# Kernel optimization log

Measured on AMD Instinct MI355X. Metric: run time of the kernel, lower is better.

The kernel has to match this reference:

```python
import jax, jax.numpy as jnp
import numpy as np

QLEN, MLEN, BSZ = 1024, 1024, 4
D_MODEL, N_HEAD, D_HEAD, D_INNER = 1024, 16, 64, 4096
KLEN = QLEN + MLEN  # = rlen
LN_EPS = 1e-5


def setup_inputs() -> dict:
    key = jax.random.key(0)
    ks = jax.random.split(key, 16)
    s = 0.02
    nhd = N_HEAD * D_HEAD
    inp = {
        "dec_inp": jax.random.normal(ks[0], (QLEN, BSZ, D_MODEL), jnp.float32),
        "r": jax.random.normal(ks[1], (KLEN, D_MODEL), jnp.float32),
        "r_w_bias": jax.random.normal(ks[2], (N_HEAD, D_HEAD), jnp.float32) * s,
        "r_r_bias": jax.random.normal(ks[3], (N_HEAD, D_HEAD), jnp.float32) * s,
        "mems": jax.random.normal(ks[4], (MLEN, BSZ, D_MODEL), jnp.float32),
        # causal mask with memory: position j visible to query i iff j <= i + MLEN
        "dec_attn_mask": (jnp.arange(KLEN)[None, :] > (jnp.arange(QLEN)[:, None] + MLEN))[:, :, None],
        # parameters
        "qkv_w": jax.random.normal(ks[5], (D_MODEL, 3 * nhd), jnp.float32) * s,
        "r_w": jax.random.normal(ks[6], (D_MODEL, nhd), jnp.float32) * s,
        "o_w": jax.random.normal(ks[7], (nhd, D_MODEL), jnp.float32) * s,
        "ln1_w": jnp.ones((D_MODEL,), jnp.float32),
        "ln1_b": jnp.zeros((D_MODEL,), jnp.float32),
        "ln2_w": jnp.ones((D_MODEL,), jnp.float32),
        "ln2_b": jnp.zeros((D_MODEL,), jnp.float32),
        "ff_w1": jax.random.normal(ks[8], (D_MODEL, D_INNER), jnp.float32) * s,
        "ff_b1": jnp.zeros((D_INNER,), jnp.float32),
        "ff_w2": jax.random.normal(ks[9], (D_INNER, D_MODEL), jnp.float32) * s,
        "ff_b2": jnp.zeros((D_MODEL,), jnp.float32),
    }
    return inp


def _layer_norm(x, w, b):
    mu = jnp.mean(x, axis=-1, keepdims=True)
    var = jnp.mean(jnp.square(x - mu), axis=-1, keepdims=True)
    return (x - mu) * jax.lax.rsqrt(var + LN_EPS) * w + b


def _rel_shift(x):
    # x: [qlen, rlen, bsz, n_head] -- Transformer-XL pad/reshape shift
    q, rl = x.shape[0], x.shape[1]
    zero_pad = jnp.zeros((q, 1) + x.shape[2:], x.dtype)
    x_padded = jnp.concatenate([zero_pad, x], axis=1)
    x_padded = x_padded.reshape((rl + 1, q) + x.shape[2:])
    return x_padded[1:].reshape(x.shape)


def reference(dec_inp, r, r_w_bias, r_r_bias, mems, dec_attn_mask,
              qkv_w, r_w, o_w, ln1_w, ln1_b, ln2_w, ln2_b,
              ff_w1, ff_b1, ff_w2, ff_b2):
    qlen, bsz = dec_inp.shape[0], dec_inp.shape[1]
    nhd = N_HEAD * D_HEAD
    scale = 1.0 / (D_HEAD ** 0.5)

    cat = jnp.concatenate([mems, dec_inp], axis=0)          # [klen, b, d]
    w_heads = cat @ qkv_w                                   # [klen, b, 3*nhd]
    w_head_q, w_head_k, w_head_v = jnp.split(w_heads, 3, axis=-1)
    w_head_q = w_head_q[-qlen:]                             # [qlen, b, nhd]
    klen = w_head_k.shape[0]

    w_head_q = w_head_q.reshape(qlen, bsz, N_HEAD, D_HEAD)
    w_head_k = w_head_k.reshape(klen, bsz, N_HEAD, D_HEAD)
    w_head_v = w_head_v.reshape(klen, bsz, N_HEAD, D_HEAD)
    r_head_k = (r @ r_w).reshape(-1, N_HEAD, D_HEAD)        # [rlen, n, d]

    AC = jnp.einsum('ibnd,jbnd->ijbn', w_head_q + r_w_bias, w_head_k)
    BD = jnp.einsum('ibnd,jnd->ijbn', w_head_q + r_r_bias, r_head_k)
    BD = _rel_shift(BD)

    attn_score = (AC + BD) * scale                          # [q, k, b, n]
    attn_score = jnp.where(dec_attn_mask[:, :, :, None], -jnp.inf, attn_score)
    attn_prob = jax.nn.softmax(attn_score, axis=1)

    attn_vec = jnp.einsum('ijbn,jbnd->ibnd', attn_prob, w_head_v)
    attn_out = attn_vec.reshape(qlen, bsz, nhd) @ o_w       # [q, b, d]

    output = _layer_norm(dec_inp + attn_out, ln1_w, ln1_b)
    ff = jax.nn.relu(output @ ff_w1 + ff_b1) @ ff_w2 + ff_b2
    return _layer_norm(output + ff, ln2_w, ln2_b)
```

## Files before the change

kernel.cpp:

```cpp
#include <hip/hip_runtime.h>
#include <hip/hip_bf16.h>
#include <math.h>

#define QLEN 1024
#define MLEN 1024
#define BSZ 4
#define KLEN 2048
#define NH 16
#define DH 64
#define DM 1024
#define DI 4096
#define NHD 1024
#define LN_EPS 1e-5f

typedef short bf16x8 __attribute__((ext_vector_type(8)));
typedef float f32x4 __attribute__((ext_vector_type(4)));
typedef unsigned int uint4v __attribute__((ext_vector_type(4)));

__device__ __forceinline__ float bf2f(unsigned short u) {
    union { unsigned u32; float f; } x; x.u32 = ((unsigned)u) << 16; return x.f;
}
__device__ __forceinline__ unsigned short f2bf(float f) {
    __hip_bfloat16 h = __float2bfloat16(f);
    return *(unsigned short*)&h;
}

static const size_t OFF_CATB  = 0;
static const size_t OFF_VTG   = 0;
static const size_t OFF_WHB   = 16777216;
static const size_t OFF_RB    = 67108864;
static const size_t OFF_RHKB  = 71303168;
static const size_t OFF_AVB   = 75497472;
static const size_t OFF_TMPB  = 83886080;
static const size_t OFF_ML    = 92274688;
static const size_t OFF_LN1B  = 117440512;
static const size_t OFF_FFHB  = 125829120;
static const size_t OFF_QKVWT = 159383552;
static const size_t OFF_RWT   = 165675008;
static const size_t OFF_OWT   = 167772160;
static const size_t OFF_FFW1T = 169869312;
static const size_t OFF_FFW2T = 178257920;

__global__ __launch_bounds__(256) void cast_cat(const float* __restrict__ mems,
                                                const float* __restrict__ dec,
                                                unsigned short* __restrict__ out) {
    size_t i8 = ((size_t)blockIdx.x * 256 + threadIdx.x) * 8;
    const size_t half = (size_t)MLEN * BSZ * DM;
    const float* src = (i8 < half) ? (mems + i8) : (dec + (i8 - half));
    float4 v0 = *(const float4*)src;
    float4 v1 = *(const float4*)(src + 4);
    ushort4 o0 = {f2bf(v0.x), f2bf(v0.y), f2bf(v0.z), f2bf(v0.w)};
    ushort4 o1 = {f2bf(v1.x), f2bf(v1.y), f2bf(v1.z), f2bf(v1.w)};
    *(ushort4*)&out[i8] = o0;
    *(ushort4*)&out[i8 + 4] = o1;
}

__global__ __launch_bounds__(256) void cast_f32_bf16(const float* __restrict__ in,
                                                     unsigned short* __restrict__ out) {
    size_t i8 = ((size_t)blockIdx.x * 256 + threadIdx.x) * 8;
    float4 v0 = *(const float4*)(in + i8);
    float4 v1 = *(const float4*)(in + i8 + 4);
    ushort4 o0 = {f2bf(v0.x), f2bf(v0.y), f2bf(v0.z), f2bf(v0.w)};
    ushort4 o1 = {f2bf(v1.x), f2bf(v1.y), f2bf(v1.z), f2bf(v1.w)};
    *(ushort4*)&out[i8] = o0;
    *(ushort4*)&out[i8 + 4] = o1;
}

__global__ __launch_bounds__(256) void transpose_cast_all(
        const float* __restrict__ qkv_w, const float* __restrict__ r_w,
        const float* __restrict__ o_w,  const float* __restrict__ ff_w1,
        const float* __restrict__ ff_w2,
        unsigned short* __restrict__ qkvwT, unsigned short* __restrict__ rwT,
        unsigned short* __restrict__ owT, unsigned short* __restrict__ ffw1T,
        unsigned short* __restrict__ ffw2T) {
    __shared__ float tile[32][33];
    const int bid = blockIdx.x;
    const float* in; unsigned short* out; int K, N, nx, lid;
    if (bid < 3072)      { in = qkv_w; out = qkvwT; K = 1024; N = 3072; nx = 96;  lid = bid; }
    else if (bid < 4096) { in = r_w;   out = rwT;   K = 1024; N = 1024; nx = 32;  lid = bid - 3072; }
    else if (bid < 5120) { in = o_w;   out = owT;   K = 1024; N = 1024; nx = 32;  lid = bid - 4096; }
    else if (bid < 9216) { in = ff_w1; out = ffw1T; K = 1024; N = 4096; nx = 128; lid = bid - 5120; }
    else                 { in = ff_w2; out = ffw2T; K = 4096; N = 1024; nx = 32;  lid = bid - 9216; }
    const int n0 = (lid % nx) * 32;
    const int k0 = (lid / nx) * 32;
    const int t = threadIdx.x;
    const int r = t >> 3;
    const int c0 = (t & 7) << 2;
    float4 v = *(const float4*)&in[(size_t)(k0 + r) * N + n0 + c0];
    tile[r][c0 + 0] = v.x; tile[r][c0 + 1] = v.y;
    tile[r][c0 + 2] = v.z; tile[r][c0 + 3] = v.w;
    __syncthreads();
    ushort4 o = {f2bf(tile[c0 + 0][r]), f2bf(tile[c0 + 1][r]),
                 f2bf(tile[c0 + 2][r]), f2bf(tile[c0 + 3][r])};
    *(ushort4*)&out[(size_t)(n0 + r) * K + k0 + c0] = o;
}

__global__ __launch_bounds__(256) void gemm_bf16(const unsigned short* __restrict__ A,
                                                 const unsigned short* __restrict__ Bt,
                                                 const float* __restrict__ bias,
                                                 void* __restrict__ C,
                                                 int M, int N, int K, int flags) {
    __shared__ __align__(16) unsigned short As[128 * 64];
    __shared__ __align__(16) unsigned short Bs[128 * 64];

    const int tid = threadIdx.x;
    const int w = tid >> 6, l = tid & 63;
    const int wr = w >> 1, wc = w & 1;
    const int row0 = blockIdx.y * 128;
    const int col0 = blockIdx.x * 128;

    f32x4 acc[4][4] = {};

    uint4v ra[4], rb[4];
    {
#pragma unroll
        for (int q = 0; q < 4; ++q) {
            int f = q * 256 + tid, r = f >> 3, c = f & 7;
            ra[q] = *(const uint4v*)&A[(size_t)(row0 + r) * K + c * 8];
            rb[q] = *(const uint4v*)&Bt[(size_t)(col0 + r) * K + c * 8];
        }
    }

    const int nt = K >> 6;
    for (int kt = 0; kt < nt; ++kt) {
        __syncthreads();
#pragma unroll
        for (int q = 0; q < 4; ++q) {
            int f = q * 256 + tid, r = f >> 3, c = f & 7;
            int sw = (c ^ (r & 7)) << 3;
            *(uint4v*)&As[r * 64 + sw] = ra[q];
            *(uint4v*)&Bs[r * 64 + sw] = rb[q];
        }
        __syncthreads();
        if (kt + 1 < nt) {
            const int k0 = (kt + 1) << 6;
#pragma unroll
            for (int q = 0; q < 4; ++q) {
                int f = q * 256 + tid, r = f >> 3, c = f & 7;
                ra[q] = *(const uint4v*)&A[(size_t)(row0 + r) * K + k0 + c * 8];
                rb[q] = *(const uint4v*)&Bt[(size_t)(col0 + r) * K + k0 + c * 8];
            }
        }
#pragma unroll
        for (int ks = 0; ks < 2; ++ks) {
            bf16x8 a[4], bfr[4];
#pragma unroll
            for (int m = 0; m < 4; ++m) {
                int arow = wr * 64 + m * 16 + (l & 15);
                int chunk = (ks * 4 + (l >> 4)) ^ (arow & 7);
                a[m] = *(const bf16x8*)&As[arow * 64 + chunk * 8];
            }
#pragma unroll
            for (int n = 0; n < 4; ++n) {
                int brow = wc * 64 + n * 16 + (l & 15);
                int chunk = (ks * 4 + (l >> 4)) ^ (brow & 7);
                bfr[n] = *(const bf16x8*)&Bs[brow * 64 + chunk * 8];
            }
#pragma unroll
            for (int m = 0; m < 4; ++m)
#pragma unroll
                for (int n = 0; n < 4; ++n)
                    acc[m][n] = __builtin_amdgcn_mfma_f32_16x16x32_bf16(a[m], bfr[n], acc[m][n], 0, 0, 0);
        }
    }

#pragma unroll
    for (int n = 0; n < 4; ++n) {
        const int ccol = col0 + wc * 64 + n * 16 + (l & 15);
        const float bv = (flags & 1) ? bias[ccol] : 0.0f;
#pragma unroll
        for (int m = 0; m < 4; ++m) {
            const int crow0 = row0 + wr * 64 + m * 16 + ((l >> 4) << 2);
#pragma unroll
            for (int reg = 0; reg < 4; ++reg) {
                float v = acc[m][n][reg] + bv;
                if (flags & 2) v = fmaxf(v, 0.0f);
                if (flags & 4)
                    ((unsigned short*)C)[(size_t)(crow0 + reg) * N + ccol] = f2bf(v);
                else
                    ((float*)C)[(size_t)(crow0 + reg) * N + ccol] = v;
            }
        }
    }
}

__global__ __launch_bounds__(256) void gemm_bf16_64(const unsigned short* __restrict__ A,
                                                    const unsigned short* __restrict__ Bt,
                                                    const float* __restrict__ bias,
                                                    void* __restrict__ C,
                                                    int M, int N, int K, int flags) {
    __shared__ __align__(16) unsigned short As[64 * 64];
    __shared__ __align__(16) unsigned short Bs[64 * 64];

    const int tid = threadIdx.x;
    const int w = tid >> 6, l = tid & 63;
    const int wr = w >> 1, wc = w & 1;
    const int row0 = blockIdx.y * 64;
    const int col0 = blockIdx.x * 64;

    f32x4 acc[2][2] = {};

    uint4v ra[2], rb[2];
    {
#pragma unroll
        for (int q = 0; q < 2; ++q) {
            int f = q * 256 + tid, r = f >> 3, c = f & 7;
            ra[q] = *(const uint4v*)&A[(size_t)(row0 + r) * K + c * 8];
            rb[q] = *(const uint4v*)&Bt[(size_t)(col0 + r) * K + c * 8];
        }
    }

    const int nt = K >> 6;
    for (int kt = 0; kt < nt; ++kt) {
        __syncthreads();
#pragma unroll
        for (int q = 0; q < 2; ++q) {
            int f = q * 256 + tid, r = f >> 3, c = f & 7;
            int sw = (c ^ (r & 7)) << 3;
            *(uint4v*)&As[r * 64 + sw] = ra[q];
            *(uint4v*)&Bs[r * 64 + sw] = rb[q];
        }
        __syncthreads();
        if (kt + 1 < nt) {
            const int k0 = (kt + 1) << 6;
#pragma unroll
            for (int q = 0; q < 2; ++q) {
                int f = q * 256 + tid, r = f >> 3, c = f & 7;
                ra[q] = *(const uint4v*)&A[(size_t)(row0 + r) * K + k0 + c * 8];
                rb[q] = *(const uint4v*)&Bt[(size_t)(col0 + r) * K + k0 + c * 8];
            }
        }
#pragma unroll
        for (int ks = 0; ks < 2; ++ks) {
            bf16x8 a[2], bfr[2];
#pragma unroll
            for (int m = 0; m < 2; ++m) {
                int arow = wr * 32 + m * 16 + (l & 15);
                int chunk = (ks * 4 + (l >> 4)) ^ (arow & 7);
                a[m] = *(const bf16x8*)&As[arow * 64 + chunk * 8];
            }
#pragma unroll
            for (int n = 0; n < 2; ++n) {
                int brow = wc * 32 + n * 16 + (l & 15);
                int chunk = (ks * 4 + (l >> 4)) ^ (brow & 7);
                bfr[n] = *(const bf16x8*)&Bs[brow * 64 + chunk * 8];
            }
#pragma unroll
            for (int m = 0; m < 2; ++m)
#pragma unroll
                for (int n = 0; n < 2; ++n)
                    acc[m][n] = __builtin_amdgcn_mfma_f32_16x16x32_bf16(a[m], bfr[n], acc[m][n], 0, 0, 0);
        }
    }

#pragma unroll
    for (int n = 0; n < 2; ++n) {
        const int ccol = col0 + wc * 32 + n * 16 + (l & 15);
        const float bv = (flags & 1) ? bias[ccol] : 0.0f;
#pragma unroll
        for (int m = 0; m < 2; ++m) {
            const int crow0 = row0 + wr * 32 + m * 16 + ((l >> 4) << 2);
#pragma unroll
            for (int reg = 0; reg < 4; ++reg) {
                float v = acc[m][n][reg] + bv;
                if (flags & 2) v = fmaxf(v, 0.0f);
                if (flags & 4)
                    ((unsigned short*)C)[(size_t)(crow0 + reg) * N + ccol] = f2bf(v);
                else
                    ((float*)C)[(size_t)(crow0 + reg) * N + ccol] = v;
            }
        }
    }
}

__global__ __launch_bounds__(256) void vtrans(const unsigned short* __restrict__ whb,
                                              unsigned short* __restrict__ vtg) {
    __shared__ unsigned short tile[64][72];
    const int bn = blockIdx.y;
    const int b = bn >> 4, n = bn & 15, nb = n * 64;
    const int jt0 = blockIdx.x * 64;
    const int tid = threadIdx.x;
#pragma unroll
    for (int g = 0; g < 2; ++g) {
        int f = g * 256 + tid;
        int key = f >> 3, c = f & 7;
        uint4v v = *(const uint4v*)&whb[((size_t)(jt0 + key) * 4 + b) * 3072 + 2048 + nb + c * 8];
        *(uint4v*)&tile[key][c * 8] = v;
    }
    __syncthreads();
#pragma unroll
    for (int g = 0; g < 2; ++g) {
        int f = g * 256 + tid;
        int d = f >> 3, ck = f & 7;
        unsigned short tmp[8];
#pragma unroll
        for (int e = 0; e < 8; ++e) tmp[e] = tile[ck * 8 + e][d];
        *(uint4v*)&vtg[(size_t)bn * 131072 + (size_t)d * 2048 + jt0 + ck * 8] = *(uint4v*)tmp;
    }
}

__global__ __launch_bounds__(512) void flash_attn_mfma(const unsigned short* __restrict__ whb,
                                                       const unsigned short* __restrict__ rhkb,
                                                       const unsigned short* __restrict__ vtg,
                                                       const float* __restrict__ r_w_bias,
                                                       const float* __restrict__ r_r_bias,
                                                       float* __restrict__ opart,
                                                       float* __restrict__ ml) {
    const int bid = blockIdx.x;
    const int bn = bid >> 3;
    const int kk0 = bid & 7;
    const int b = bn >> 4, n = bn & 15, nb = n * 64;
    const int tid = threadIdx.x;
    const int wq = tid >> 6;
    const int lane = tid & 63;
    const int rg = lane >> 4;
    const int lc = lane & 15;
    const int m7 = lc & 7;
    const float QSCALE = 0.125f * 1.44269504089f;

    __shared__ __align__(16) unsigned short Ks[4096];
    __shared__ __align__(16) unsigned short Rs[16384];
    __shared__ __align__(16) unsigned short Vt[4096];
    __shared__ __align__(16) unsigned short SCR[8][1440];

    const int wbase_off = 112 - 16 * wq;
    const int srow = tid >> 3;
    const int sc = tid & 7;
    unsigned short* scr = &SCR[wq][0];

#pragma unroll 1
    for (int job = 0; job < 2; ++job) {
        const int h = job;
        const int bx = job ? (7 - kk0) : kk0;
        const int i0 = bx << 7;
        const int halfn = bx + 9;
        const int kt0 = h * halfn;
        const int ktend = kt0 + halfn;

        bf16x8 qac0, qac1, qbd0, qbd1;
        {
            const int qrow = MLEN + i0 + wq * 16 + lc;
            const unsigned short* qp = whb + ((size_t)qrow * 4 + b) * 3072 + nb + rg * 8;
            bf16x8 q0 = *(const bf16x8*)(qp);
            bf16x8 q1 = *(const bf16x8*)(qp + 32);
            const float* wbp = r_w_bias + nb + rg * 8;
            const float* rbp = r_r_bias + nb + rg * 8;
#pragma unroll
            for (int e = 0; e < 8; ++e) {
                const float v0 = bf2f((unsigned short)q0[e]);
                const float v1 = bf2f((unsigned short)q1[e]);
                qac0[e] = (short)f2bf((v0 + wbp[e]) * QSCALE);
                qbd0[e] = (short)f2bf((v0 + rbp[e]) * QSCALE);
                qac1[e] = (short)f2bf((v1 + wbp[32 + e]) * QSCALE);
                qbd1[e] = (short)f2bf((v1 + rbp[32 + e]) * QSCALE);
            }
        }

        f32x4 Oacc[4] = {};
        float mrun = -INFINITY, lrun = 0.f;

        uint4v pk, pv, pr3[3];
        {
            const int j0 = kt0 << 6;
            pk = *(const uint4v*)&whb[((size_t)(j0 + srow) * 4 + b) * 3072 + 1024 + nb + sc * 8];
            pv = *(const uint4v*)&vtg[(size_t)bn * 131072 + (size_t)srow * 2048 + j0 + sc * 8];
            const int relst = j0 - i0 + 896;
#pragma unroll
            for (int p = 0; p < 3; ++p) {
                int a = relst + p * 64 + srow;
                if (a > 2047) a = 2047;
                pr3[p] = *(const uint4v*)&rhkb[(size_t)a * 1024 + nb + sc * 8];
            }
        }

        for (int kt = kt0; kt < ktend; ++kt) {
            const int jt0 = kt << 6;
            const int relbase = jt0 - i0 + 896;
            __syncthreads();

            *(uint4v*)&Ks[srow * 64 + ((sc ^ (srow & 7)) << 3)] = pk;
            *(uint4v*)&Vt[srow * 64 + ((sc ^ (srow & 7)) << 3)] = pv;
            if (kt == kt0) {
#pragma unroll
                for (int p = 0; p < 3; ++p) {
                    int a = relbase + p * 64 + srow;
                    if (a > 2047) a = 2047;
                    const int dst = ((a >> 6) & 3) * 4096 + (a & 63) * 64 + ((sc ^ (a & 7)) << 3);
                    *(uint4v*)&Rs[dst] = pr3[p];
                }
            } else {
                int a = relbase + 128 + srow;
                if (a > 2047) a = 2047;
                const int dst = ((a >> 6) & 3) * 4096 + (a & 63) * 64 + ((sc ^ (a & 7)) << 3);
                *(uint4v*)&Rs[dst] = pr3[0];
            }
            if (kt + 1 < ktend) {
                const int jn = jt0 + 64;
                pk = *(const uint4v*)&whb[((size_t)(jn + srow) * 4 + b) * 3072 + 1024 + nb + sc * 8];
                pv = *(const uint4v*)&vtg[(size_t)bn * 131072 + (size_t)srow * 2048 + jn + sc * 8];
                int a = relbase + 192 + srow;
                if (a > 2047) a = 2047;
                pr3[0] = *(const uint4v*)&rhkb[(size_t)a * 1024 + nb + sc * 8];
            }
            __syncthreads();

            f32x4 S[4];
            __builtin_amdgcn_s_setprio(1);
#pragma unroll
            for (int nf = 0; nf < 4; ++nf) {
                const int row = nf * 16 + lc;
                const bf16x8 kf0 = *(const bf16x8*)&Ks[row * 64 + ((rg ^ m7) << 3)];
                const bf16x8 kf1 = *(const bf16x8*)&Ks[row * 64 + (((4 + rg) ^ m7) << 3)];
                f32x4 zz = {0.f, 0.f, 0.f, 0.f};
                zz = __builtin_amdgcn_mfma_f32_16x16x32_bf16(kf0, qac0, zz, 0, 0, 0);
                S[nf] = __builtin_amdgcn_mfma_f32_16x16x32_bf16(kf1, qac1, zz, 0, 0, 0);
            }
            __builtin_amdgcn_s_setprio(0);

            const int wbase = relbase + wbase_off;
#pragma unroll
            for (int g = 0; g < 5; ++g) {
                const int a = wbase + g * 16 + lc;
                const int rbase = ((a >> 6) & 3) * 4096 + (a & 63) * 64;
                const bf16x8 rf0 = *(const bf16x8*)&Rs[rbase + ((rg ^ m7) << 3)];
                const bf16x8 rf1 = *(const bf16x8*)&Rs[rbase + (((4 + rg) ^ m7) << 3)];
                f32x4 bd = {0.f, 0.f, 0.f, 0.f};
                bd = __builtin_amdgcn_mfma_f32_16x16x32_bf16(rf0, qbd0, bd, 0, 0, 0);
                bd = __builtin_amdgcn_mfma_f32_16x16x32_bf16(rf1, qbd1, bd, 0, 0, 0);
                const int wrow = g * 16 + rg * 4;
#pragma unroll
                for (int r = 0; r < 4; ++r)
                    scr[(wrow + r) * 18 + lc] = f2bf(bd[r]);
            }

            const bool needmask = (wbase + 78 > 2047);
            float tmax = -INFINITY;
#pragma unroll
            for (int nf = 0; nf < 4; ++nf) {
#pragma unroll
                for (int r = 0; r < 4; ++r) {
                    const int wb_ = 15 + nf * 16 + rg * 4 + r - lc;
                    float s = S[nf][r] + bf2f(scr[wb_ * 18 + lc]);
                    if (needmask) s = (wbase + wb_ <= 2047) ? s : -INFINITY;
                    S[nf][r] = s;
                    tmax = fmaxf(tmax, s);
                }
            }

            tmax = fmaxf(tmax, __shfl_xor(tmax, 16));
            tmax = fmaxf(tmax, __shfl_xor(tmax, 32));
            const float mn = fmaxf(mrun, tmax);
            const float ef = __builtin_amdgcn_exp2f(mrun - mn);
            mrun = mn;
            float rsum = 0.f;
#pragma unroll
            for (int nf = 0; nf < 4; ++nf) {
#pragma unroll
                for (int r = 0; r < 4; ++r) {
                    const float p = __builtin_amdgcn_exp2f(S[nf][r] - mn);
                    S[nf][r] = p;
                    rsum += p;
                }
            }
            rsum += __shfl_xor(rsum, 16);
            rsum += __shfl_xor(rsum, 32);
            lrun = lrun * ef + rsum;
            if (__any(ef < 1.0f)) {
#pragma unroll
                for (int nf = 0; nf < 4; ++nf)
#pragma unroll
                    for (int r = 0; r < 4; ++r) Oacc[nf][r] *= ef;
            }

#pragma unroll
            for (int nf = 0; nf < 4; ++nf) {
                ushort4 pw = {f2bf(S[nf][0]), f2bf(S[nf][1]), f2bf(S[nf][2]), f2bf(S[nf][3])};
                const int chunk = nf * 2 + (rg >> 1);
                *(ushort4*)&scr[lc * 64 + ((chunk ^ m7) << 3) + ((rg & 1) << 2)] = pw;
            }

            {
                const bf16x8 pf0 = *(const bf16x8*)&scr[lc * 64 + ((rg ^ m7) << 3)];
                const bf16x8 pf1 = *(const bf16x8*)&scr[lc * 64 + (((4 + rg) ^ m7) << 3)];
                __builtin_amdgcn_s_setprio(1);
#pragma unroll
                for (int nf = 0; nf < 4; ++nf) {
                    const int row = nf * 16 + lc;
                    const bf16x8 vf0 = *(const bf16x8*)&Vt[row * 64 + ((rg ^ m7) << 3)];
                    const bf16x8 vf1 = *(const bf16x8*)&Vt[row * 64 + (((4 + rg) ^ m7) << 3)];
                    Oacc[nf] = __builtin_amdgcn_mfma_f32_16x16x32_bf16(vf0, pf0, Oacc[nf], 0, 0, 0);
                    Oacc[nf] = __builtin_amdgcn_mfma_f32_16x16x32_bf16(vf1, pf1, Oacc[nf], 0, 0, 0);
                }
                __builtin_amdgcn_s_setprio(0);
            }
        }

        const int qg = i0 + wq * 16 + lc;
        const int rowf = qg * 4 + b;
        float* op = opart + (size_t)h * 4194304 + (size_t)rowf * 1024 + nb;
#pragma unroll
        for (int nf = 0; nf < 4; ++nf) {
            float4 o = {Oacc[nf][0], Oacc[nf][1], Oacc[nf][2], Oacc[nf][3]};
            *(float4*)&op[nf * 16 + rg * 4] = o;
        }
        if (rg == 0) {
            float* mp = ml + (size_t)h * 131072 + ((size_t)rowf * 16 + n) * 2;
            mp[0] = mrun;
            mp[1] = lrun;
        }
    }
}

__global__ __launch_bounds__(256) void merge_attn(const float* __restrict__ opart,
                                                  const float* __restrict__ ml,
                                                  unsigned short* __restrict__ avb) {
    const size_t g = (size_t)blockIdx.x * 256 + threadIdx.x;
    const size_t c8 = g << 3;
    const int row = (int)(c8 >> 10);
    const int col = (int)(c8 & 1023);
    const int n = col >> 6;
    const size_t mlb = ((size_t)row * 16 + n) * 2;
    const float m1 = ml[mlb], l1 = ml[mlb + 1];
    const float m2 = ml[131072 + mlb], l2 = ml[131072 + mlb + 1];
    const float m = fmaxf(m1, m2);
    const float e1 = __builtin_amdgcn_exp2f(m1 - m), e2 = __builtin_amdgcn_exp2f(m2 - m);
    const float inv = 1.0f / (e1 * l1 + e2 * l2);
    const float s1 = e1 * inv, s2 = e2 * inv;
    const float4 oa1 = *(const float4*)&opart[c8];
    const float4 ob1 = *(const float4*)&opart[c8 + 4];
    const float4 oa2 = *(const float4*)&opart[4194304 + c8];
    const float4 ob2 = *(const float4*)&opart[4194304 + c8 + 4];
    ushort4 oa = {f2bf(oa1.x * s1 + oa2.x * s2), f2bf(oa1.y * s1 + oa2.y * s2),
                  f2bf(oa1.z * s1 + oa2.z * s2), f2bf(oa1.w * s1 + oa2.w * s2)};
    ushort4 ob = {f2bf(ob1.x * s1 + ob2.x * s2), f2bf(ob1.y * s1 + ob2.y * s2),
                  f2bf(ob1.z * s1 + ob2.z * s2), f2bf(ob1.w * s1 + ob2.w * s2)};
    *(ushort4*)&avb[c8] = oa;
    *(ushort4*)&avb[c8 + 4] = ob;
}

__global__ __launch_bounds__(256) void add_ln_kernel(const float* __restrict__ a,
                                                     const unsigned short* __restrict__ b,
                                                     const float* __restrict__ w,
                                                     const float* __restrict__ bias,
                                                     unsigned short* __restrict__ out_bf) {
    const int row = blockIdx.x;
    const int t = threadIdx.x;
    const int c0 = t << 2;
    __shared__ float red[256];

    const float4 av = *(const float4*)&a[(size_t)row * DM + c0];
    const ushort4 bu = *(const ushort4*)&b[(size_t)row * DM + c0];
    float x0 = av.x + bf2f(bu.x), x1 = av.y + bf2f(bu.y);
    float x2 = av.z + bf2f(bu.z), x3 = av.w + bf2f(bu.w);

    red[t] = x0 + x1 + x2 + x3;
    __syncthreads();
    for (int off = 128; off > 0; off >>= 1) {
        if (t < off) red[t] += red[t + off];
        __syncthreads();
    }
    const float mu = red[0] * (1.0f / DM);
    __syncthreads();

    const float d0 = x0 - mu, d1 = x1 - mu, d2 = x2 - mu, d3 = x3 - mu;
    red[t] = d0 * d0 + d1 * d1 + d2 * d2 + d3 * d3;
    __syncthreads();
    for (int off = 128; off > 0; off >>= 1) {
        if (t < off) red[t] += red[t + off];
        __syncthreads();
    }
    const float rstd = rsqrtf(red[0] * (1.0f / DM) + LN_EPS);

    const float4 wv = *(const float4*)&w[c0];
    const float4 bsv = *(const float4*)&bias[c0];
    ushort4 ob = {f2bf(d0 * rstd * wv.x + bsv.x), f2bf(d1 * rstd * wv.y + bsv.y),
                  f2bf(d2 * rstd * wv.z + bsv.z), f2bf(d3 * rstd * wv.w + bsv.w)};
    *(ushort4*)&out_bf[(size_t)row * DM + c0] = ob;
}

__global__ __launch_bounds__(256) void add_ln2_kernel(const unsigned short* __restrict__ a,
                                                      const unsigned short* __restrict__ b,
                                                      const float* __restrict__ w,
                                                      const float* __restrict__ bias,
                                                      float* __restrict__ out) {
    const int row = blockIdx.x;
    const int t = threadIdx.x;
    const int c0 = t << 2;
    __shared__ float red[256];

    const ushort4 au = *(const ushort4*)&a[(size_t)row * DM + c0];
    const ushort4 bu = *(const ushort4*)&b[(size_t)row * DM + c0];
    float x0 = bf2f(au.x) + bf2f(bu.x), x1 = bf2f(au.y) + bf2f(bu.y);
    float x2 = bf2f(au.z) + bf2f(bu.z), x3 = bf2f(au.w) + bf2f(bu.w);

    red[t] = x0 + x1 + x2 + x3;
    __syncthreads();
    for (int off = 128; off > 0; off >>= 1) {
        if (t < off) red[t] += red[t + off];
        __syncthreads();
    }
    const float mu = red[0] * (1.0f / DM);
    __syncthreads();

    const float d0 = x0 - mu, d1 = x1 - mu, d2 = x2 - mu, d3 = x3 - mu;
    red[t] = d0 * d0 + d1 * d1 + d2 * d2 + d3 * d3;
    __syncthreads();
    for (int off = 128; off > 0; off >>= 1) {
        if (t < off) red[t] += red[t + off];
        __syncthreads();
    }
    const float rstd = rsqrtf(red[0] * (1.0f / DM) + LN_EPS);

    const float4 wv = *(const float4*)&w[c0];
    const float4 bsv = *(const float4*)&bias[c0];
    float4 o = {d0 * rstd * wv.x + bsv.x, d1 * rstd * wv.y + bsv.y,
                d2 * rstd * wv.z + bsv.z, d3 * rstd * wv.w + bsv.w};
    *(float4*)&out[(size_t)row * DM + c0] = o;
}

extern "C" void kernel_launch(void* const* d_in, const int* in_sizes, int n_in,
                              void* d_out, int out_size, void* d_ws, size_t ws_size,
                              hipStream_t stream) {
    const float* dec_inp  = (const float*)d_in[0];
    const float* r        = (const float*)d_in[1];
    const float* r_w_bias = (const float*)d_in[2];
    const float* r_r_bias = (const float*)d_in[3];
    const float* mems     = (const float*)d_in[4];
    const float* qkv_w    = (const float*)d_in[6];
    const float* r_w      = (const float*)d_in[7];
    const float* o_w      = (const float*)d_in[8];
    const float* ln1_w    = (const float*)d_in[9];
    const float* ln1_b    = (const float*)d_in[10];
    const float* ln2_w    = (const float*)d_in[11];
    const float* ln2_b    = (const float*)d_in[12];
    const float* ff_w1    = (const float*)d_in[13];
    const float* ff_b1    = (const float*)d_in[14];
    const float* ff_w2    = (const float*)d_in[15];
    const float* ff_b2    = (const float*)d_in[16];
    float* out = (float*)d_out;
    char* ws = (char*)d_ws;

    unsigned short* catb  = (unsigned short*)(ws + OFF_CATB);
    unsigned short* vtg   = (unsigned short*)(ws + OFF_VTG);
    unsigned short* whb   = (unsigned short*)(ws + OFF_WHB);
    unsigned short* rb    = (unsigned short*)(ws + OFF_RB);
    unsigned short* rhkb  = (unsigned short*)(ws + OFF_RHKB);
    unsigned short* avb   = (unsigned short*)(ws + OFF_AVB);
    unsigned short* tmpb  = (unsigned short*)(ws + OFF_TMPB);
    float*          mlbuf = (float*)(ws + OFF_ML);
    unsigned short* ln1b  = (unsigned short*)(ws + OFF_LN1B);
    unsigned short* ffhb  = (unsigned short*)(ws + OFF_FFHB);
    float*          opart = (float*)(ws + OFF_FFHB);
    unsigned short* qkvwT = (unsigned short*)(ws + OFF_QKVWT);
    unsigned short* rwT   = (unsigned short*)(ws + OFF_RWT);
    unsigned short* owT   = (unsigned short*)(ws + OFF_OWT);
    unsigned short* ffw1T = (unsigned short*)(ws + OFF_FFW1T);
    unsigned short* ffw2T = (unsigned short*)(ws + OFF_FFW2T);

    cast_cat<<<dim3(4096), 256, 0, stream>>>(mems, dec_inp, catb);
    cast_f32_bf16<<<dim3(1024), 256, 0, stream>>>(r, rb);
    transpose_cast_all<<<dim3(13312), 256, 0, stream>>>(
        qkv_w, r_w, o_w, ff_w1, ff_w2, qkvwT, rwT, owT, ffw1T, ffw2T);

    gemm_bf16<<<dim3(24, 64), 256, 0, stream>>>(catb, qkvwT, nullptr, whb,
                                                KLEN * BSZ, 3 * NHD, DM, 4);
    gemm_bf16_64<<<dim3(16, 32), 256, 0, stream>>>(rb, rwT, nullptr, rhkb,
                                                   KLEN, NHD, DM, 4);

    vtrans<<<dim3(32, 64), 256, 0, stream>>>(whb, vtg);

    flash_attn_mfma<<<dim3(512), 512, 0, stream>>>(
        whb, rhkb, vtg, r_w_bias, r_r_bias, opart, mlbuf);
    merge_attn<<<dim3(2048), 256, 0, stream>>>(opart, mlbuf, avb);

    gemm_bf16_64<<<dim3(16, 64), 256, 0, stream>>>(avb, owT, nullptr, tmpb,
                                                   QLEN * BSZ, DM, NHD, 4);
    add_ln_kernel<<<dim3(QLEN * BSZ), 256, 0, stream>>>(
        dec_inp, tmpb, ln1_w, ln1_b, ln1b);
    gemm_bf16<<<dim3(32, 32), 256, 0, stream>>>(ln1b, ffw1T, ff_b1, ffhb,
                                                QLEN * BSZ, DI, DM, 1 | 2 | 4);
    gemm_bf16_64<<<dim3(16, 64), 256, 0, stream>>>(ffhb, ffw2T, ff_b2, tmpb,
                                                   QLEN * BSZ, DM, DI, 1 | 4);
    add_ln2_kernel<<<dim3(QLEN * BSZ), 256, 0, stream>>>(
        ln1b, tmpb, ln2_w, ln2_b, out);
}
```

Measured before the change: 363.0 us.

## Add double-buffered direct-to-LDS GEMM and use it for QKV and FFN projections

Adds a 128x128-tile bf16 MFMA GEMM that loads A and B tiles straight into LDS with global_load_lds and double-buffers them, so the next K-tile's loads overlap the current tile's MFMAs. The QKV and FF1 GEMMs switch to it, and FF2 moves from the 64x64 kernel to 128x128 tiles (256 blocks). The LDS layout has no swizzle, so fragment reads may hit bank conflicts. FF2 now launches far fewer blocks, which could leave some CUs idle.

```diff
diff --git a/kernel.cpp b/kernel.cpp
--- a/kernel.cpp
+++ b/kernel.cpp
@@ -23,6 +23,10 @@
 __device__ __forceinline__ unsigned short f2bf(float f) {
     __hip_bfloat16 h = __float2bfloat16(f);
     return *(unsigned short*)&h;
+}
+__device__ __forceinline__ void gload16(const void* g, void* l) {
+    __builtin_amdgcn_global_load_lds((const __attribute__((address_space(1))) unsigned int*)g,
+                                     (__attribute__((address_space(3))) unsigned int*)l, 16, 0, 0);
 }
 
 static const size_t OFF_CATB  = 0;
@@ -184,6 +188,90 @@
     }
 }
 
+__global__ __launch_bounds__(256) void gemm_bf16_p(const unsigned short* __restrict__ A,
+                                                   const unsigned short* __restrict__ Bt,
+                                                   const float* __restrict__ bias,
+                                                   void* __restrict__ C,
+                                                   int M, int N, int K, int flags) {
+    __shared__ __align__(16) unsigned short As[2][128 * 64];
+    __shared__ __align__(16) unsigned short Bs[2][128 * 64];
+
+    const int tid = threadIdx.x;
+    const int w = tid >> 6, l = tid & 63;
+    const int wr = w >> 1, wc = w & 1;
+    const int row0 = blockIdx.y * 128;
+    const int col0 = blockIdx.x * 128;
+    const int r32 = tid >> 3;
+    const int c8 = tid & 7;
+
+    f32x4 acc[4][4] = {};
+    const int nt = K >> 6;
+
+#pragma unroll
+    for (int q = 0; q < 4; ++q) {
+        const int row = q * 32 + r32;
+        gload16(&A[(size_t)(row0 + row) * K + c8 * 8], &As[0][row * 64 + c8 * 8]);
+        gload16(&Bt[(size_t)(col0 + row) * K + c8 * 8], &Bs[0][row * 64 + c8 * 8]);
+    }
+    asm volatile("s_waitcnt vmcnt(0)" ::: "memory");
+    __builtin_amdgcn_s_barrier();
+
+    int cur = 0;
+#pragma unroll 1
+    for (int kt = 0; kt < nt; ++kt) {
+        if (kt + 1 < nt) {
+            const int k0 = (kt + 1) << 6;
+#pragma unroll
+            for (int q = 0; q < 4; ++q) {
+                const int row = q * 32 + r32;
+                gload16(&A[(size_t)(row0 + row) * K + k0 + c8 * 8], &As[cur ^ 1][row * 64 + c8 * 8]);
+                gload16(&Bt[(size_t)(col0 + row) * K + k0 + c8 * 8], &Bs[cur ^ 1][row * 64 + c8 * 8]);
+            }
+        }
+#pragma unroll
+        for (int ks = 0; ks < 2; ++ks) {
+            bf16x8 a[4], bfr[4];
+#pragma unroll
+            for (int m = 0; m < 4; ++m) {
+                const int arow = wr * 64 + m * 16 + (l & 15);
+                a[m] = *(const bf16x8*)&As[cur][arow * 64 + ks * 32 + (l >> 4) * 8];
+            }
+#pragma unroll
+            for (int n = 0; n < 4; ++n) {
+                const int brow = wc * 64 + n * 16 + (l & 15);
+                bfr[n] = *(const bf16x8*)&Bs[cur][brow * 64 + ks * 32 + (l >> 4) * 8];
+            }
+#pragma unroll
+            for (int m = 0; m < 4; ++m)
+#pragma unroll
+                for (int n = 0; n < 4; ++n)
+                    acc[m][n] = __builtin_amdgcn_mfma_f32_16x16x32_bf16(a[m], bfr[n], acc[m][n], 0, 0, 0);
+        }
+        asm volatile("s_waitcnt vmcnt(0)" ::: "memory");
+        __builtin_amdgcn_s_barrier();
+        cur ^= 1;
+    }
+
+#pragma unroll
+    for (int n = 0; n < 4; ++n) {
+        const int ccol = col0 + wc * 64 + n * 16 + (l & 15);
+        const float bv = (flags & 1) ? bias[ccol] : 0.0f;
+#pragma unroll
+        for (int m = 0; m < 4; ++m) {
+            const int crow0 = row0 + wr * 64 + m * 16 + ((l >> 4) << 2);
+#pragma unroll
+            for (int reg = 0; reg < 4; ++reg) {
+                float v = acc[m][n][reg] + bv;
+                if (flags & 2) v = fmaxf(v, 0.0f);
+                if (flags & 4)
+                    ((unsigned short*)C)[(size_t)(crow0 + reg) * N + ccol] = f2bf(v);
+                else
+                    ((float*)C)[(size_t)(crow0 + reg) * N + ccol] = v;
+            }
+        }
+    }
+}
+
 __global__ __launch_bounds__(256) void gemm_bf16_64(const unsigned short* __restrict__ A,
                                                     const unsigned short* __restrict__ Bt,
                                                     const float* __restrict__ bias,
@@ -662,8 +750,8 @@
     transpose_cast_all<<<dim3(13312), 256, 0, stream>>>(
         qkv_w, r_w, o_w, ff_w1, ff_w2, qkvwT, rwT, owT, ffw1T, ffw2T);
 
-    gemm_bf16<<<dim3(24, 64), 256, 0, stream>>>(catb, qkvwT, nullptr, whb,
-                                                KLEN * BSZ, 3 * NHD, DM, 4);
+    gemm_bf16_p<<<dim3(24, 64), 256, 0, stream>>>(catb, qkvwT, nullptr, whb,
+                                                  KLEN * BSZ, 3 * NHD, DM, 4);
     gemm_bf16_64<<<dim3(16, 32), 256, 0, stream>>>(rb, rwT, nullptr, rhkb,
                                                    KLEN, NHD, DM, 4);
 
@@ -677,10 +765,10 @@
                                                    QLEN * BSZ, DM, NHD, 4);
     add_ln_kernel<<<dim3(QLEN * BSZ), 256, 0, stream>>>(
         dec_inp, tmpb, ln1_w, ln1_b, ln1b);
-    gemm_bf16<<<dim3(32, 32), 256, 0, stream>>>(ln1b, ffw1T, ff_b1, ffhb,
-                                                QLEN * BSZ, DI, DM, 1 | 2 | 4);
-    gemm_bf16_64<<<dim3(16, 64), 256, 0, stream>>>(ffhb, ffw2T, ff_b2, tmpb,
-                                                   QLEN * BSZ, DM, DI, 1 | 4);
+    gemm_bf16_p<<<dim3(32, 32), 256, 0, stream>>>(ln1b, ffw1T, ff_b1, ffhb,
+                                                  QLEN * BSZ, DI, DM, 1 | 2 | 4);
+    gemm_bf16_p<<<dim3(8, 32), 256, 0, stream>>>(ffhb, ffw2T, ff_b2, tmpb,
+                                                 QLEN * BSZ, DM, DI, 1 | 4);
     add_ln2_kernel<<<dim3(QLEN * BSZ), 256, 0, stream>>>(
         ln1b, tmpb, ln2_w, ln2_b, out);
 }
```

Result: slower. 411.1 us (+13.3%).
